# Kernel optimization log

Measured on AMD Instinct MI355X. Metric: run time of the kernel, lower is better.

Reference implementation:

```python
import jax, jax.numpy as jnp
import numpy as np

N = 50000          # nodes
E = 1600000        # edges (avg degree 32)
H = 64             # hidden dim (module default x=64)
C = 10             # num_classes = max(y)+1
SLOPE = 0.01       # torch leaky_relu default


def _glorot(key, shape):
    lim = jnp.sqrt(6.0 / (shape[0] + shape[1]))
    return jax.random.uniform(key, shape, jnp.float32, -lim, lim)


def setup_inputs() -> dict:
    key = jax.random.key(0)
    ks = jax.random.split(key, 8)
    x = jax.random.normal(ks[0], (N, 1), jnp.float32)
    edge_index = jax.random.randint(ks[1], (2, E), 0, N, dtype=jnp.int64)
    W1 = _glorot(ks[2], (1, 10));  b1 = jnp.zeros((10,), jnp.float32)
    W2 = _glorot(ks[3], (10, H));  b2 = jnp.zeros((H,), jnp.float32)
    W3 = _glorot(ks[4], (H, H));   b3 = jnp.zeros((H,), jnp.float32)
    fcW = _glorot(ks[5], (H * N, C))
    fcb = jnp.zeros((C,), jnp.float32)
    return {"x": x, "edge_index": edge_index, "W1": W1, "b1": b1,
            "W2": W2, "b2": b2, "W3": W3, "b3": b3, "fcW": fcW, "fcb": fcb}


def _gcn_layer(h, W, b, src, dst, norm):
    # GCNConv: out = D^{-1/2} (A + I) D^{-1/2} (h W) + b
    h = h @ W                                   # [N, out]
    msg = h[src] * norm[:, None]                # gather + edge-scale
    agg = jax.ops.segment_sum(msg, dst, num_segments=N)  # scatter-add
    return agg + b


def reference(x, edge_index, W1, b1, W2, b2, W3, b3, fcW, fcb):
    src, dst = edge_index[0], edge_index[1]
    loop = jnp.arange(N, dtype=src.dtype)
    src_all = jnp.concatenate([src, loop])      # add self-loops
    dst_all = jnp.concatenate([dst, loop])
    deg = jax.ops.segment_sum(jnp.ones_like(dst_all, jnp.float32), dst_all,
                              num_segments=N)   # >= 1 due to self-loops
    dinv = jax.lax.rsqrt(deg)
    norm = dinv[src_all] * dinv[dst_all]        # per-edge normalization

    h = jax.nn.leaky_relu(_gcn_layer(x, W1, b1, src_all, dst_all, norm), SLOPE)
    h = jax.nn.leaky_relu(_gcn_layer(h, W2, b2, src_all, dst_all, norm), SLOPE)
    h = jax.nn.leaky_relu(_gcn_layer(h, W3, b3, src_all, dst_all, norm), SLOPE)

    logits = h.reshape(-1) @ fcW + fcb          # [C]
    return jax.nn.softmax(logits, axis=0)
```

## Files before the change

kernel.cpp:

```cpp
#include <hip/hip_runtime.h>
#include <hip/hip_fp16.h>
#include <hip/hip_fp8.h>


constexpr int F1  = 10;
constexpr int F1P = 16;
constexpr int HD  = 64;
constexpr int NC  = 10;
constexpr int LOGIT_BLOCKS = 2048;

constexpr int BSH   = 7;
constexpr int NBC   = 391;
constexpr int BCAPG = 5120;
constexpr int CSTR  = 16;
constexpr int LCAP  = 38;
constexpr int TILE  = 8192;

static __device__ __forceinline__ float lrelu(float v) {
    return v > 0.0f ? v : 0.01f * v;
}

#if defined(__has_builtin)
#if __has_builtin(__builtin_amdgcn_cvt_f32_fp8)
#define FP8_DECODE(w, c) __builtin_amdgcn_cvt_f32_fp8((int)(w), (c))
#endif
#endif
#ifndef FP8_DECODE
static __device__ __forceinline__ float fp8_decode_sw(unsigned w, int c) {
    __hip_fp8_e4m3 t; t.__x = (unsigned char)(w >> (8 * c)); return (float)t;
}
#define FP8_DECODE(w, c) fp8_decode_sw((w), (c))
#endif

static __device__ __forceinline__ unsigned char fp8_encode(float v) {
    __hip_fp8_e4m3 t(v);
    return (unsigned char)t.__x;
}

__global__ void k_bcur(int* __restrict__ bcur, int NB) {
    int b = blockIdx.x * blockDim.x + threadIdx.x;
    if (b < NB) bcur[b * CSTR] = b * BCAPG;
}

__global__ __launch_bounds__(512) void k_bucket(const int* __restrict__ src,
                                                const int* __restrict__ dst,
                                                int* __restrict__ bcur,
                                                unsigned* __restrict__ bpairs, int E) {
    __shared__ unsigned stage[NBC * LCAP];
    __shared__ int lcnt[NBC];
    for (int i = threadIdx.x; i < NBC; i += 512) lcnt[i] = 0;
    __syncthreads();
    int tile0 = blockIdx.x * TILE;
#pragma unroll
    for (int k = 0; k < TILE / 512; ++k) {
        int e = tile0 + k * 512 + threadIdx.x;
        if (e < E) {
            int d = dst[e];
            unsigned pk = (unsigned)src[e] | ((unsigned)(d & 127) << 16);
            int bb = d >> BSH;
            int pos = atomicAdd(&lcnt[bb], 1);
            if (pos < LCAP) stage[bb * LCAP + pos] = pk;
            else {
                int gp = atomicAdd(&bcur[bb * CSTR], 1);
                bpairs[gp] = pk;
            }
        }
    }
    __syncthreads();
    int wid = threadIdx.x >> 6, lane = threadIdx.x & 63;
    for (int bb = wid; bb < NBC; bb += 8) {
        int cntb = min(lcnt[bb], LCAP);
        if (cntb == 0) continue;
        int gp = 0;
        if (lane == 0) gp = atomicAdd(&bcur[bb * CSTR], cntb);
        gp = __shfl(gp, 0, 64);
        for (int i = lane; i < cntb; i += 64) bpairs[gp + i] = stage[bb * LCAP + i];
    }
}

__global__ __launch_bounds__(256) void k_fine(const int* __restrict__ bcur,
                                              const unsigned* __restrict__ bpairs,
                                              const float* __restrict__ x,
                                              unsigned short* __restrict__ csr,
                                              float* __restrict__ dinv,
                                              float* __restrict__ xs,
                                              int* __restrict__ rowbeg,
                                              int* __restrict__ rowend, int N) {
    __shared__ unsigned short lout[BCAPG];
    __shared__ int lcnt[128], lbeg[128];
    int b = blockIdx.x;
    int n0 = b << BSH;
    int nn = min(128, N - n0);
    int base = b * BCAPG;
    int nedges = bcur[b * CSTR] - base;
    for (int i = threadIdx.x; i < nn; i += 256) lcnt[i] = 0;
    __syncthreads();
    for (int i = threadIdx.x; i < nedges; i += 256)
        atomicAdd(&lcnt[(bpairs[base + i] >> 16) & 127], 1);
    __syncthreads();
    if (threadIdx.x == 0) {
        int acc = 0;
        for (int j = 0; j < nn; ++j) { lbeg[j] = acc; acc += lcnt[j]; }
    }
    __syncthreads();
    for (int i = threadIdx.x; i < nn; i += 256) {
        int node = n0 + i;
        float di = rsqrtf(1.0f + (float)lcnt[i]);
        dinv[node]   = di;
        xs[node]     = x[node] * di;
        rowbeg[node] = base + lbeg[i];
        rowend[node] = base + lbeg[i] + lcnt[i];
    }
    __syncthreads();
    for (int i = threadIdx.x; i < nn; i += 256) lcnt[i] = lbeg[i];
    __syncthreads();
    for (int i = threadIdx.x; i < nedges; i += 256) {
        unsigned p = bpairs[base + i];
        int pos = atomicAdd(&lcnt[(p >> 16) & 127], 1);
        lout[pos] = (unsigned short)(p & 0xFFFFu);
    }
    __syncthreads();
    for (int i = threadIdx.x; i < nedges; i += 256) csr[base + i] = lout[i];
}

__global__ void k_l1h1(const int* __restrict__ rowbeg, const int* __restrict__ rowend,
                       const unsigned short* __restrict__ csr,
                       const float* __restrict__ xs, const float* __restrict__ dinv,
                       const float* __restrict__ W1, const float* __restrict__ b1,
                       __half* __restrict__ h1s, int N) {
    int node = (blockIdx.x * blockDim.x + threadIdx.x) >> 6;
    int lane = threadIdx.x & 63;
    if (node >= N) return;
    int lo = rowbeg[node], hi = rowend[node];
    float acc = 0.0f;
    for (int j = lo + lane; j < hi; j += 64) acc += xs[csr[j]];
#pragma unroll
    for (int off = 32; off > 0; off >>= 1) acc += __shfl_xor(acc, off, 64);
    float di = dinv[node];
    float s = di * (acc + xs[node]);
    if (lane < F1P) {
        float h = (lane < F1) ? lrelu(s * W1[lane] + b1[lane]) * di : 0.0f;
        h1s[node * F1P + lane] = __float2half(h);
    }
}

__global__ __launch_bounds__(256, 4) void k_l2h2(const int* __restrict__ rowbeg,
                                                 const int* __restrict__ rowend,
                                                 const unsigned short* __restrict__ csr,
                                                 const __half* __restrict__ h1s,
                                                 const float* __restrict__ dinv,
                                                 const float* __restrict__ W2,
                                                 const float* __restrict__ b2,
                                                 unsigned char* __restrict__ h2s8, int N) {
    __shared__ float awork[4][12];
    int node = (blockIdx.x * blockDim.x + threadIdx.x) >> 6;
    int wid  = threadIdx.x >> 6;
    int lane = threadIdx.x & 63;
    bool valid = node < N;
    float w2r[F1];
#pragma unroll
    for (int k = 0; k < F1; ++k) w2r[k] = W2[k * HD + lane];
    int g = lane >> 3, f2 = lane & 7;
    int lo = 0, deg = 0;
    if (valid) { lo = rowbeg[node]; deg = rowend[node] - lo; }
    int myidx = (lane < deg) ? (int)csr[lo + lane] : 0;
    int nfull = min(deg, 64);
    float a0 = 0.0f, a1 = 0.0f;
#pragma unroll
    for (int j = 0; j < 64; j += 8) {
        int e = j + g;
        int sn = __shfl(myidx, e, 64);
        if (e < nfull) {
            __half2 hv = *reinterpret_cast<const __half2*>(h1s + sn * F1P + f2 * 2);
            a0 += __low2float(hv);
            a1 += __high2float(hv);
        }
    }
    for (int j = 64; j < deg; j += 8) {
        int e = j + g;
        if (e < deg) {
            int sn = csr[lo + e];
            __half2 hv = *reinterpret_cast<const __half2*>(h1s + sn * F1P + f2 * 2);
            a0 += __low2float(hv);
            a1 += __high2float(hv);
        }
    }
    a0 += __shfl_xor(a0, 8, 64); a0 += __shfl_xor(a0, 16, 64); a0 += __shfl_xor(a0, 32, 64);
    a1 += __shfl_xor(a1, 8, 64); a1 += __shfl_xor(a1, 16, 64); a1 += __shfl_xor(a1, 32, 64);
    if (valid) {
        __half2 hs = *reinterpret_cast<const __half2*>(h1s + node * F1P + f2 * 2);
        a0 += __low2float(hs);
        a1 += __high2float(hs);
    }
    if (g == 0 && f2 < 5)
        *reinterpret_cast<float2*>(&awork[wid][f2 * 2]) = make_float2(a0, a1);
    __syncthreads();
    float4 av0 = *reinterpret_cast<const float4*>(&awork[wid][0]);
    float4 av1 = *reinterpret_cast<const float4*>(&awork[wid][4]);
    float2 av2 = *reinterpret_cast<const float2*>(&awork[wid][8]);
    float S = av0.x * w2r[0] + av0.y * w2r[1] + av0.z * w2r[2] + av0.w * w2r[3]
            + av1.x * w2r[4] + av1.y * w2r[5] + av1.z * w2r[6] + av1.w * w2r[7]
            + av2.x * w2r[8] + av2.y * w2r[9];
    if (valid) {
        float di = dinv[node];
        h2s8[node * HD + lane] = fp8_encode(lrelu(di * S + b2[lane]) * di);
    }
}

__global__ __launch_bounds__(256, 4) void k_l3h3(const int* __restrict__ rowbeg,
                                                 const int* __restrict__ rowend,
                                                 const unsigned short* __restrict__ csr,
                                                 const unsigned char* __restrict__ h2s8,
                                                 const float* __restrict__ dinv,
                                                 const float* __restrict__ W3,
                                                 const float* __restrict__ b3,
                                                 float* __restrict__ h3, int N) {
    __shared__ float awork[4][HD];
    int node = (blockIdx.x * blockDim.x + threadIdx.x) >> 6;
    int wid  = threadIdx.x >> 6;
    int lane = threadIdx.x & 63;
    bool valid = node < N;
    float w3r[HD];
#pragma unroll
    for (int k = 0; k < HD; ++k) w3r[k] = W3[k * HD + lane];
    int g = lane >> 4, q = lane & 15;
    int lo = 0, deg = 0;
    if (valid) { lo = rowbeg[node]; deg = rowend[node] - lo; }
    int myidx = (lane < deg) ? (int)csr[lo + lane] : 0;
    int nfull = min(deg, 64);
    float a0 = 0.0f, a1 = 0.0f, a2 = 0.0f, a3 = 0.0f;
#pragma unroll
    for (int j = 0; j < 64; j += 4) {
        int e = j + g;
        int sn = __shfl(myidx, e, 64);
        if (e < nfull) {
            unsigned wv = *reinterpret_cast<const unsigned*>(h2s8 + sn * HD + q * 4);
            a0 += FP8_DECODE(wv, 0);
            a1 += FP8_DECODE(wv, 1);
            a2 += FP8_DECODE(wv, 2);
            a3 += FP8_DECODE(wv, 3);
        }
    }
    for (int j = 64; j < deg; j += 4) {
        int e = j + g;
        if (e < deg) {
            int sn = csr[lo + e];
            unsigned wv = *reinterpret_cast<const unsigned*>(h2s8 + sn * HD + q * 4);
            a0 += FP8_DECODE(wv, 0);
            a1 += FP8_DECODE(wv, 1);
            a2 += FP8_DECODE(wv, 2);
            a3 += FP8_DECODE(wv, 3);
        }
    }
    a0 += __shfl_xor(a0, 16, 64); a0 += __shfl_xor(a0, 32, 64);
    a1 += __shfl_xor(a1, 16, 64); a1 += __shfl_xor(a1, 32, 64);
    a2 += __shfl_xor(a2, 16, 64); a2 += __shfl_xor(a2, 32, 64);
    a3 += __shfl_xor(a3, 16, 64); a3 += __shfl_xor(a3, 32, 64);
    if (valid) {
        unsigned ws = *reinterpret_cast<const unsigned*>(h2s8 + node * HD + q * 4);
        a0 += FP8_DECODE(ws, 0);
        a1 += FP8_DECODE(ws, 1);
        a2 += FP8_DECODE(ws, 2);
        a3 += FP8_DECODE(ws, 3);
    }
    if (g == 0)
        *reinterpret_cast<float4*>(&awork[wid][q * 4]) = make_float4(a0, a1, a2, a3);
    __syncthreads();
    float S = 0.0f;
#pragma unroll
    for (int c = 0; c < 16; ++c) {
        float4 av = *reinterpret_cast<const float4*>(&awork[wid][c * 4]);
        S += av.x * w3r[4 * c]     + av.y * w3r[4 * c + 1]
           + av.z * w3r[4 * c + 2] + av.w * w3r[4 * c + 3];
    }
    if (valid) {
        float di = dinv[node];
        h3[node * HD + lane] = lrelu(di * S + b3[lane]);
    }
}

__global__ void k_logits_part(const float* __restrict__ h3,
                              const float4* __restrict__ fw4,
                              float* __restrict__ partial, int P ) {
    float acc[NC];
#pragma unroll
    for (int c = 0; c < NC; ++c) acc[c] = 0.0f;
    int nth = gridDim.x * blockDim.x;
    for (int p = blockIdx.x * blockDim.x + threadIdx.x; p < P; p += nth) {
        const float4* w = fw4 + (size_t)p * 5;
        float4 w0 = w[0], w1 = w[1], w2 = w[2], w3 = w[3], w4 = w[4];
        float2 hv = *reinterpret_cast<const float2*>(h3 + 2 * (size_t)p);
        acc[0] += hv.x * w0.x; acc[1] += hv.x * w0.y; acc[2] += hv.x * w0.z; acc[3] += hv.x * w0.w;
        acc[4] += hv.x * w1.x; acc[5] += hv.x * w1.y; acc[6] += hv.x * w1.z; acc[7] += hv.x * w1.w;
        acc[8] += hv.x * w2.x; acc[9] += hv.x * w2.y; acc[0] += hv.y * w2.z; acc[1] += hv.y * w2.w;
        acc[2] += hv.y * w3.x; acc[3] += hv.y * w3.y; acc[4] += hv.y * w3.z; acc[5] += hv.y * w3.w;
        acc[6] += hv.y * w4.x; acc[7] += hv.y * w4.y; acc[8] += hv.y * w4.z; acc[9] += hv.y * w4.w;
    }
#pragma unroll
    for (int c = 0; c < NC; ++c) {
        float v = acc[c];
#pragma unroll
        for (int off = 32; off > 0; off >>= 1) v += __shfl_down(v, off, 64);
        acc[c] = v;
    }
    __shared__ float ls[4][NC];
    int wid = threadIdx.x >> 6, lane = threadIdx.x & 63;
    if (lane == 0) {
#pragma unroll
        for (int c = 0; c < NC; ++c) ls[wid][c] = acc[c];
    }
    __syncthreads();
    if (threadIdx.x < NC) {
        float ssum = ls[0][threadIdx.x] + ls[1][threadIdx.x]
                   + ls[2][threadIdx.x] + ls[3][threadIdx.x];
        partial[blockIdx.x * NC + threadIdx.x] = ssum;
    }
}

__global__ void k_final(const float* __restrict__ partial, int nblk,
                        const float* __restrict__ fcb, float* __restrict__ out) {
    __shared__ float ls[NC];
    if (threadIdx.x < NC) ls[threadIdx.x] = 0.0f;
    __syncthreads();
    const int NCHUNK = 256 / NC;
    int c = threadIdx.x % NC;
    int chunk = threadIdx.x / NC;
    float ssum = 0.0f;
    if (chunk < NCHUNK)
        for (int i = chunk; i < nblk; i += NCHUNK) ssum += partial[i * NC + c];
    if (chunk < NCHUNK) atomicAdd(&ls[c], ssum);
    __syncthreads();
    if (threadIdx.x == 0) {
        float l[NC], m = -1e30f;
        for (int k = 0; k < NC; ++k) { l[k] = ls[k] + fcb[k]; m = fmaxf(m, l[k]); }
        float sum = 0.0f;
        for (int k = 0; k < NC; ++k) { l[k] = expf(l[k] - m); sum += l[k]; }
        float inv = 1.0f / sum;
        for (int k = 0; k < NC; ++k) out[k] = l[k] * inv;
    }
}

extern "C" void kernel_launch(void* const* d_in, const int* in_sizes, int n_in,
                              void* d_out, int out_size, void* d_ws, size_t ws_size,
                              hipStream_t stream) {
    const float* x   = (const float*)d_in[0];
    const int*   ei  = (const int*)d_in[1];
    const float* W1  = (const float*)d_in[2];
    const float* b1  = (const float*)d_in[3];
    const float* W2  = (const float*)d_in[4];
    const float* b2  = (const float*)d_in[5];
    const float* W3  = (const float*)d_in[6];
    const float* b3  = (const float*)d_in[7];
    const float* fcW = (const float*)d_in[8];
    const float* fcb = (const float*)d_in[9];
    float* out = (float*)d_out;

    const int N = in_sizes[0];
    const int E = in_sizes[1] / 2;
    const int* src = ei;
    const int* dst = ei + E;
    const int NB = (N + 127) >> BSH;

    char* w = (char*)d_ws;
    auto take = [&](size_t elems) { void* p = w; w += elems * 4; return p; };
    float* dinv    = (float*)take(N);
    int*   rowbeg  = (int*)  take(N);
    int*   rowend  = (int*)  take(N);
    int*   bcur    = (int*)  take((size_t)NB * CSTR);
    unsigned short* csr = (unsigned short*)take((size_t)NB * BCAPG / 2);
    float* xs      = (float*)take(N);
    __half* h1s    = (__half*)take((size_t)N * F1P / 2);
    unsigned char* h2s8 = (unsigned char*)take((size_t)N * HD / 4);
    float* h3      = (float*)take((size_t)N * HD);
    float* partial = xs;
    unsigned* bpairs = (unsigned*)h3;

    const int B = 256;
    auto cdiv = [](long long a, long long b) { return (int)((a + b - 1) / b); };

    k_bcur  <<<cdiv(NB, B), B, 0, stream>>>(bcur, NB);
    k_bucket<<<cdiv(E, TILE), 512, 0, stream>>>(src, dst, bcur, bpairs, E);
    k_fine  <<<NB, 256, 0, stream>>>(bcur, bpairs, x, csr, dinv, xs, rowbeg, rowend, N);

    k_l1h1<<<cdiv((long long)N * 64, B), B, 0, stream>>>(rowbeg, rowend, csr, xs, dinv, W1, b1, h1s, N);
    k_l2h2<<<cdiv((long long)N * 64, B), B, 0, stream>>>(rowbeg, rowend, csr, h1s, dinv, W2, b2, h2s8, N);
    k_l3h3<<<cdiv((long long)N * 64, B), B, 0, stream>>>(rowbeg, rowend, csr, h2s8, dinv, W3, b3, h3, N);

    const int P = (N * HD) / 2;
    k_logits_part<<<LOGIT_BLOCKS, B, 0, stream>>>(h3, (const float4*)fcW, partial, P);
    k_final<<<1, 256, 0, stream>>>(partial, LOGIT_BLOCKS, fcb, out);
}
```

Before: 191.7 us.

## Fuse final classifier dot product into layer-3 kernel and drop h3 buffer

Layer 3 now multiplies each node's activations directly with its slice of fcW and reduces the results to per-block partial logits. This removes the 12.8 MB h3 write and re-read and one kernel launch. fcW is prefetched with nontemporal double loads at kernel start so that the load overlaps the gather. In exchange, register pressure rises (launch bounds drop to 3 blocks per SM) and there are many more partials (12500 blocks), so the final reduction now runs with 1024 threads.

After: 225.7 us. 1.18x slower.

```diff
diff --git a/kernel.cpp b/kernel.cpp
--- a/kernel.cpp
+++ b/kernel.cpp
@@ -7,7 +7,6 @@
 constexpr int F1P = 16;
 constexpr int HD  = 64;
 constexpr int NC  = 10;
-constexpr int LOGIT_BLOCKS = 2048;
 
 constexpr int BSH   = 7;
 constexpr int NBC   = 391;
@@ -207,15 +206,17 @@
     }
 }
 
-__global__ __launch_bounds__(256, 4) void k_l3h3(const int* __restrict__ rowbeg,
+__global__ __launch_bounds__(256, 3) void k_l3fc(const int* __restrict__ rowbeg,
                                                  const int* __restrict__ rowend,
                                                  const unsigned short* __restrict__ csr,
                                                  const unsigned char* __restrict__ h2s8,
                                                  const float* __restrict__ dinv,
                                                  const float* __restrict__ W3,
                                                  const float* __restrict__ b3,
-                                                 float* __restrict__ h3, int N) {
+                                                 const float* __restrict__ fcW,
+                                                 float* __restrict__ partial, int N) {
     __shared__ float awork[4][HD];
+    __shared__ float ls[4][NC];
     int node = (blockIdx.x * blockDim.x + threadIdx.x) >> 6;
     int wid  = threadIdx.x >> 6;
     int lane = threadIdx.x & 63;
@@ -223,6 +224,15 @@
     float w3r[HD];
 #pragma unroll
     for (int k = 0; k < HD; ++k) w3r[k] = W3[k * HD + lane];
+    double fw_d[5];
+    if (valid) {
+        const double* fw = reinterpret_cast<const double*>(fcW + (size_t)(node * HD + lane) * NC);
+#pragma unroll
+        for (int c = 0; c < 5; ++c) fw_d[c] = __builtin_nontemporal_load(fw + c);
+    } else {
+#pragma unroll
+        for (int c = 0; c < 5; ++c) fw_d[c] = 0.0;
+    }
     int g = lane >> 4, q = lane & 15;
     int lo = 0, deg = 0;
     if (valid) { lo = rowbeg[node]; deg = rowend[node] - lo; }
@@ -273,28 +283,17 @@
         S += av.x * w3r[4 * c]     + av.y * w3r[4 * c + 1]
            + av.z * w3r[4 * c + 2] + av.w * w3r[4 * c + 3];
     }
+    float h = 0.0f;
     if (valid) {
         float di = dinv[node];
-        h3[node * HD + lane] = lrelu(di * S + b3[lane]);
-    }
-}
-
-__global__ void k_logits_part(const float* __restrict__ h3,
-                              const float4* __restrict__ fw4,
-                              float* __restrict__ partial, int P ) {
+        h = lrelu(di * S + b3[lane]);
+    }
     float acc[NC];
 #pragma unroll
-    for (int c = 0; c < NC; ++c) acc[c] = 0.0f;
-    int nth = gridDim.x * blockDim.x;
-    for (int p = blockIdx.x * blockDim.x + threadIdx.x; p < P; p += nth) {
-        const float4* w = fw4 + (size_t)p * 5;
-        float4 w0 = w[0], w1 = w[1], w2 = w[2], w3 = w[3], w4 = w[4];
-        float2 hv = *reinterpret_cast<const float2*>(h3 + 2 * (size_t)p);
-        acc[0] += hv.x * w0.x; acc[1] += hv.x * w0.y; acc[2] += hv.x * w0.z; acc[3] += hv.x * w0.w;
-        acc[4] += hv.x * w1.x; acc[5] += hv.x * w1.y; acc[6] += hv.x * w1.z; acc[7] += hv.x * w1.w;
-        acc[8] += hv.x * w2.x; acc[9] += hv.x * w2.y; acc[0] += hv.y * w2.z; acc[1] += hv.y * w2.w;
-        acc[2] += hv.y * w3.x; acc[3] += hv.y * w3.y; acc[4] += hv.y * w3.z; acc[5] += hv.y * w3.w;
-        acc[6] += hv.y * w4.x; acc[7] += hv.y * w4.y; acc[8] += hv.y * w4.z; acc[9] += hv.y * w4.w;
+    for (int c = 0; c < 5; ++c) {
+        float2 f = *reinterpret_cast<float2*>(&fw_d[c]);
+        acc[2 * c]     = h * f.x;
+        acc[2 * c + 1] = h * f.y;
     }
 #pragma unroll
     for (int c = 0; c < NC; ++c) {
@@ -303,8 +302,6 @@
         for (int off = 32; off > 0; off >>= 1) v += __shfl_down(v, off, 64);
         acc[c] = v;
     }
-    __shared__ float ls[4][NC];
-    int wid = threadIdx.x >> 6, lane = threadIdx.x & 63;
     if (lane == 0) {
 #pragma unroll
         for (int c = 0; c < NC; ++c) ls[wid][c] = acc[c];
@@ -317,12 +314,13 @@
     }
 }
 
-__global__ void k_final(const float* __restrict__ partial, int nblk,
-                        const float* __restrict__ fcb, float* __restrict__ out) {
+__global__ __launch_bounds__(1024) void k_final(const float* __restrict__ partial, int nblk,
+                                                const float* __restrict__ fcb,
+                                                float* __restrict__ out) {
     __shared__ float ls[NC];
     if (threadIdx.x < NC) ls[threadIdx.x] = 0.0f;
     __syncthreads();
-    const int NCHUNK = 256 / NC;
+    const int NCHUNK = 1024 / NC;
     int c = threadIdx.x % NC;
     int chunk = threadIdx.x / NC;
     float ssum = 0.0f;
@@ -371,9 +369,9 @@
     float* xs      = (float*)take(N);
     __half* h1s    = (__half*)take((size_t)N * F1P / 2);
     unsigned char* h2s8 = (unsigned char*)take((size_t)N * HD / 4);
-    float* h3      = (float*)take((size_t)N * HD);
-    float* partial = xs;
-    unsigned* bpairs = (unsigned*)h3;
+    float* scratch = (float*)take((size_t)N * HD);
+    unsigned* bpairs = (unsigned*)scratch;
+    float* partial   = scratch;
 
     const int B = 256;
     auto cdiv = [](long long a, long long b) { return (int)((a + b - 1) / b); };
@@ -384,9 +382,8 @@
 
     k_l1h1<<<cdiv((long long)N * 64, B), B, 0, stream>>>(rowbeg, rowend, csr, xs, dinv, W1, b1, h1s, N);
     k_l2h2<<<cdiv((long long)N * 64, B), B, 0, stream>>>(rowbeg, rowend, csr, h1s, dinv, W2, b2, h2s8, N);
-    k_l3h3<<<cdiv((long long)N * 64, B), B, 0, stream>>>(rowbeg, rowend, csr, h2s8, dinv, W3, b3, h3, N);
-
-    const int P = (N * HD) / 2;
-    k_logits_part<<<LOGIT_BLOCKS, B, 0, stream>>>(h3, (const float4*)fcW, partial, P);
-    k_final<<<1, 256, 0, stream>>>(partial, LOGIT_BLOCKS, fcb, out);
-}
+    const int NBLK3 = cdiv((long long)N * 64, B);
+    k_l3fc<<<NBLK3, B, 0, stream>>>(rowbeg, rowend, csr, h2s8, dinv, W3, b3, fcW, partial, N);
+
+    k_final<<<1, 1024, 0, stream>>>(partial, NBLK3, fcb, out);
+}
```
